# Kernel tuning notes

Hardware: AMD Instinct MI355X
Metric: run time of the kernel (lower is better)

Reference implementation:

```python
import jax, jax.numpy as jnp
import numpy as np
from jax import lax

# Model constants (match init_kwargs)
DIM = 512
NUM_HEADS = 8
HEAD_DIM = 64
INNER = NUM_HEADS * HEAD_DIM  # 512
SCALE = HEAD_DIM ** -0.5
# CoaT ConvRelPosEnc window dict {3:2, 5:3, 7:3}: head-group sizes and kernel sizes
HEAD_SPLITS = [2, 3, 3]
KSIZES = [3, 5, 7]


def _depthwise_conv(x, w, b):
    # x: [B, Cg, H, W], w: [Cg, 1, k, k] (OIHW, depthwise), b: [Cg]
    cg = x.shape[1]
    y = lax.conv_general_dilated(
        x, w, window_strides=(1, 1), padding='SAME',
        feature_group_count=cg,
        dimension_numbers=('NCHW', 'OIHW', 'NCHW'))
    return y + b[None, :, None, None]


def setup_inputs() -> dict:
    key = jax.random.key(0)
    ks = jax.random.split(key, 10)
    B, Himg, Wimg = 16, 56, 56
    N = Himg * Wimg
    x = jax.random.normal(ks[0], (B, N, DIM), dtype=jnp.float32)
    w_qkv = jax.random.normal(ks[1], (3 * INNER, DIM), dtype=jnp.float32) * 0.02
    w_proj = jax.random.normal(ks[2], (DIM, INNER), dtype=jnp.float32) * 0.02
    b_proj = jnp.zeros((DIM,), dtype=jnp.float32)
    # depthwise conv params per head group: channels = split * HEAD_DIM
    w3 = jax.random.normal(ks[3], (2 * HEAD_DIM, 1, 3, 3), dtype=jnp.float32) * 0.02
    b3 = jnp.zeros((2 * HEAD_DIM,), dtype=jnp.float32)
    w5 = jax.random.normal(ks[4], (3 * HEAD_DIM, 1, 5, 5), dtype=jnp.float32) * 0.02
    b5 = jnp.zeros((3 * HEAD_DIM,), dtype=jnp.float32)
    w7 = jax.random.normal(ks[5], (3 * HEAD_DIM, 1, 7, 7), dtype=jnp.float32) * 0.02
    b7 = jnp.zeros((3 * HEAD_DIM,), dtype=jnp.float32)
    return {"x": x, "H": Himg, "W": Wimg,
            "w_qkv": w_qkv, "w_proj": w_proj, "b_proj": b_proj,
            "w3": w3, "b3": b3, "w5": w5, "b5": b5, "w7": w7, "b7": b7}


def reference(x, H, W, w_qkv, w_proj, b_proj, w3, b3, w5, b5, w7, b7):
    B, N, C = x.shape
    h, d = NUM_HEADS, HEAD_DIM
    qkv = x @ w_qkv.T  # [B, N, 3*INNER]
    q, k, v = jnp.split(qkv, 3, axis=-1)
    # b n (h d) -> b h n d
    def to_heads(t):
        return t.reshape(B, N, h, d).transpose(0, 2, 1, 3)
    q, k, v = to_heads(q), to_heads(k), to_heads(v)
    # factorized attention: softmax(k) over sequence dim, then two batched GEMMs
    k_softmax = jax.nn.softmax(k, axis=2)
    kv = jnp.einsum('bhnk,bhnv->bhkv', k_softmax, v)          # [B,h,d,d]
    factor_att = jnp.einsum('bhnk,bhkv->bhnv', q, kv)          # [B,h,N,d]
    # ConvRelPosEnc: depthwise conv on v (as 2D map), elementwise multiply by q
    v_img = v.transpose(0, 1, 3, 2).reshape(B, h * d, H, W)    # [B, h*d, H, W]
    c0, c1 = HEAD_SPLITS[0] * d, (HEAD_SPLITS[0] + HEAD_SPLITS[1]) * d
    conv_v = jnp.concatenate([
        _depthwise_conv(v_img[:, :c0], w3, b3),
        _depthwise_conv(v_img[:, c0:c1], w5, b5),
        _depthwise_conv(v_img[:, c1:], w7, b7),
    ], axis=1)                                                 # [B, h*d, H, W]
    conv_v = conv_v.reshape(B, h, d, N).transpose(0, 1, 3, 2)  # [B,h,N,d]
    crpe = q * conv_v
    out = SCALE * factor_att + crpe                            # [B,h,N,d]
    out = out.transpose(0, 2, 1, 3).reshape(B, N, h * d)       # b h n d -> b n (h d)
    out = out @ w_proj.T + b_proj
    return out
```

## Files before the change

kernel.cpp:

```cpp
#include <hip/hip_runtime.h>
#include <hip/hip_bf16.h>
#include <cstdint>
#include <cstddef>

using u16 = unsigned short;
using u32 = unsigned int;
using f32x4 = __attribute__((ext_vector_type(4))) float;
using bf16x8 = __attribute__((ext_vector_type(8))) short;

#define NB   16
#define NSEQ 3136
#define NH   8
#define HD   64
#define CDIM 512
#define CQKV 1536

static __device__ __forceinline__ u16 f2bf(float f) {
  u32 u = __builtin_bit_cast(u32, f);
  u = (u + 0x7FFFu + ((u >> 16) & 1u)) >> 16;
  return (u16)u;
}
static __device__ __forceinline__ float bf2f(u16 h) {
  u32 u = ((u32)h) << 16;
  return __builtin_bit_cast(float, u);
}
static __device__ __forceinline__ void async16(const void* g, void* l) {
  __builtin_amdgcn_global_load_lds((const __attribute__((address_space(1))) u32*)g,
                                   (__attribute__((address_space(3))) u32*)l, 16, 0, 0);
}

__global__ __launch_bounds__(256) void cvt_kernel(const float* __restrict__ in,
                                                  u16* __restrict__ out, int n4) {
  int i = (int)(blockIdx.x * 256 + threadIdx.x);
  if (i >= n4) return;
  f32x4 v = *(const f32x4*)(in + (size_t)i * 4);
  uint2 uu;
  uu.x = (u32)f2bf(v[0]) | ((u32)f2bf(v[1]) << 16);
  uu.y = (u32)f2bf(v[2]) | ((u32)f2bf(v[3]) << 16);
  *(uint2*)(out + (size_t)i * 4) = uu;
}

#define VMW(n) asm volatile("s_waitcnt vmcnt(" #n ")" ::: "memory")

template<bool OUT_FP32>
__global__ __launch_bounds__(512, 2) void gemm256(
    const u16* __restrict__ Ap, const u16* __restrict__ Bp, void* __restrict__ Cp,
    const float* __restrict__ bias, int K, int lda, int ldb, int ldc, int nbn)
{
  __shared__ u16 sm[2][2][2][128 * 64];
  int nwg = (int)gridDim.x;
  int bid = (int)blockIdx.x;
  int wg = (bid & 7) * (nwg >> 3) + (bid >> 3);
  int bm = wg / nbn, bn = wg - bm * nbn;
  int m0 = bm * 256, n0 = bn * 256;
  int t = (int)threadIdx.x;
  int lane = t & 63, w = t >> 6;
  int wm = w >> 2, wn = w & 3;
  int lr = lane & 15, lk = (lane >> 4) * 8;

  f32x4 acc[2][2][4][2] = {};
  bf16x8 av[4][2], bv[2][2];
  const int KT = K >> 6;

  auto stage = [&](int b, int op, int half, int kt) {
    const u16* P = op ? Bp : Ap;
    int ld = op ? ldb : lda;
    int base0 = op ? n0 : m0;
    int gc = (kt << 6) + ((((t & 7) ^ ((t >> 3) & 7))) << 3);
    #pragma unroll
    for (int rd = 0; rd < 2; ++rd) {
      int gr = base0 + half * 128 + rd * 64 + (t >> 3);
      async16(P + (size_t)gr * ld + gc, &sm[b][op][half][rd * 4096 + w * 512]);
    }
  };
  auto LOADA = [&](int b, int h) {
    #pragma unroll
    for (int mi = 0; mi < 4; ++mi)
      #pragma unroll
      for (int kk = 0; kk < 2; ++kk) {
        int r = wm * 64 + mi * 16 + lr;
        int c = kk * 32 + lk;
        av[mi][kk] = *(const bf16x8*)&sm[b][0][h][r * 64 + (c ^ ((r & 7) << 3))];
      }
  };
  auto LOADB = [&](int b, int g) {
    #pragma unroll
    for (int ni = 0; ni < 2; ++ni)
      #pragma unroll
      for (int kk = 0; kk < 2; ++kk) {
        int r = wn * 32 + ni * 16 + lr;
        int c = kk * 32 + lk;
        bv[ni][kk] = *(const bf16x8*)&sm[b][1][g][r * 64 + (c ^ ((r & 7) << 3))];
      }
  };

#define BARSEQ                                                  \
  __builtin_amdgcn_s_barrier();                                 \
  asm volatile("s_waitcnt lgkmcnt(0)" ::: "memory");            \
  __builtin_amdgcn_sched_barrier(0);                            \
  __builtin_amdgcn_s_setprio(1)
#define ENDP                                                    \
  __builtin_amdgcn_s_setprio(0);                                \
  __builtin_amdgcn_s_barrier()
#define MMQ(h_, g_)                                                          \
  _Pragma("unroll")                                                          \
  for (int kk = 0; kk < 2; ++kk) {                                           \
    _Pragma("unroll")                                                        \
    for (int mi = 0; mi < 4; ++mi) {                                         \
      _Pragma("unroll")                                                      \
      for (int ni = 0; ni < 2; ++ni)                                         \
        acc[h_][g_][mi][ni] = __builtin_amdgcn_mfma_f32_16x16x32_bf16(       \
            av[mi][kk], bv[ni][kk], acc[h_][g_][mi][ni], 0, 0, 0);           \
    }                                                                        \
  }

  stage(0, 0, 0, 0); stage(0, 1, 0, 0); stage(0, 0, 1, 0); stage(0, 1, 1, 0);
  VMW(4);
  __builtin_amdgcn_s_barrier();

  for (int kt = 0; kt < KT - 1; ++kt) {
    int bb = kt & 1;
    LOADA(bb, 0); LOADB(bb, 0);
    stage(bb ^ 1, 0, 0, kt + 1);
    VMW(2);
    BARSEQ; MMQ(0, 0); ENDP;
    LOADB(bb, 1);
    stage(bb ^ 1, 1, 0, kt + 1);
    BARSEQ; MMQ(0, 1); ENDP;
    LOADA(bb, 1);
    stage(bb ^ 1, 0, 1, kt + 1);
    BARSEQ; MMQ(1, 1); ENDP;
    LOADB(bb, 0);
    stage(bb ^ 1, 1, 1, kt + 1);
    VMW(4);
    BARSEQ; MMQ(1, 0); ENDP;
  }
  {
    int bb = (KT - 1) & 1;
    LOADA(bb, 0); LOADB(bb, 0);
    VMW(0);
    BARSEQ; MMQ(0, 0); ENDP;
    LOADB(bb, 1);
    BARSEQ; MMQ(0, 1); ENDP;
    LOADA(bb, 1);
    BARSEQ; MMQ(1, 1); ENDP;
    LOADB(bb, 0);
    BARSEQ; MMQ(1, 0); ENDP;
  }
#undef MMQ
#undef BARSEQ
#undef ENDP

  if constexpr (!OUT_FP32) {
    __syncthreads();
    u16* cs = (u16*)sm;
    #pragma unroll
    for (int h = 0; h < 2; ++h)
      #pragma unroll
      for (int g = 0; g < 2; ++g)
        #pragma unroll
        for (int mi = 0; mi < 4; ++mi)
          #pragma unroll
          for (int ni = 0; ni < 2; ++ni)
            #pragma unroll
            for (int r = 0; r < 4; ++r) {
              int row = h * 128 + wm * 64 + mi * 16 + (lane >> 4) * 4 + r;
              int col = g * 128 + wn * 32 + ni * 16 + lr;
              cs[row * 256 + (col ^ (((row >> 2) & 7) << 3))] = f2bf(acc[h][g][mi][ni][r]);
            }
    __syncthreads();
    #pragma unroll
    for (int i = 0; i < 16; ++i) {
      int e = (i * 512 + t) * 8;
      int row = e >> 8, col = e & 255;
      uint4 v = *(const uint4*)&cs[row * 256 + (col ^ (((row >> 2) & 7) << 3))];
      *(uint4*)&((u16*)Cp)[(size_t)(m0 + row) * ldc + n0 + col] = v;
    }
  } else {
    float* cf = (float*)sm;
    #pragma unroll
    for (int h = 0; h < 2; ++h) {
      __syncthreads();
      #pragma unroll
      for (int g = 0; g < 2; ++g)
        #pragma unroll
        for (int mi = 0; mi < 4; ++mi)
          #pragma unroll
          for (int ni = 0; ni < 2; ++ni)
            #pragma unroll
            for (int r = 0; r < 4; ++r) {
              int row = wm * 64 + mi * 16 + (lane >> 4) * 4 + r;
              int col = g * 128 + wn * 32 + ni * 16 + lr;
              cf[row * 256 + (col ^ (((row >> 2) & 7) << 3))] = acc[h][g][mi][ni][r];
            }
      __syncthreads();
      #pragma unroll
      for (int i = 0; i < 16; ++i) {
        int e = (i * 512 + t) * 4;
        int row = e >> 8, col = e & 255;
        f32x4 v = *(const f32x4*)&cf[row * 256 + (col ^ (((row >> 2) & 7) << 3))];
        f32x4 b4 = *(const f32x4*)&bias[n0 + col];
        v += b4;
        *(f32x4*)&((float*)Cp)[(size_t)(m0 + h * 128 + row) * ldc + n0 + col] = v;
      }
    }
  }
}

__global__ __launch_bounds__(256) void kv_partial_kernel(const u16* __restrict__ qkvb,
                                                         float* __restrict__ part) {
  int bid = (int)blockIdx.x;
  int ns = bid & 7, h = (bid >> 3) & 7, b = bid >> 6;
  int t = (int)threadIdx.x;
  int lane = t & 63, w = t >> 6;
  __shared__ float ek[56 * 64];
  __shared__ u16  vv[56 * 64];
  __shared__ float mg[64 * 64];
  int dk0 = (lane >> 3) * 8, dv0 = (lane & 7) * 8;
  float acc[8][8] = {};
  float sacc = 0.f;
  int nbase = ns * 392;
  for (int c0 = 0; c0 < 392; c0 += 56) {
    __syncthreads();
    for (int idx = t; idx < 448; idx += 256) {
      int row = idx >> 3, c8 = idx & 7;
      size_t go = (size_t)(b * NSEQ + nbase + c0 + row) * CQKV + h * HD + c8 * 8;
      uint4 kq = *(const uint4*)&qkvb[go + CDIM];
      uint4 vq = *(const uint4*)&qkvb[go + 2 * CDIM];
      const u16* kp = (const u16*)&kq;
      #pragma unroll
      for (int j = 0; j < 8; ++j)
        ek[row * 64 + c8 * 8 + j] = __expf(bf2f(kp[j]));
      *(uint4*)&vv[row * 64 + c8 * 8] = vq;
    }
    __syncthreads();
    if (w == 0) {
      #pragma unroll 4
      for (int n = 0; n < 56; ++n) sacc += ek[n * 64 + lane];
    }
    for (int n = w * 14; n < w * 14 + 14; ++n) {
      f32x4 e0 = *(const f32x4*)&ek[n * 64 + dk0];
      f32x4 e1 = *(const f32x4*)&ek[n * 64 + dk0 + 4];
      bf16x8 vq = *(const bf16x8*)&vv[n * 64 + dv0];
      float vf[8];
      #pragma unroll
      for (int j = 0; j < 8; ++j) vf[j] = bf2f((u16)vq[j]);
      #pragma unroll
      for (int i = 0; i < 4; ++i)
        #pragma unroll
        for (int j = 0; j < 8; ++j) {
          acc[i][j]     += e0[i] * vf[j];
          acc[i + 4][j] += e1[i] * vf[j];
        }
    }
  }
  __syncthreads();
  for (int wi = 0; wi < 4; ++wi) {
    if (w == wi) {
      #pragma unroll
      for (int i = 0; i < 8; ++i) {
        #pragma unroll
        for (int j4 = 0; j4 < 2; ++j4) {
          f32x4* p = (f32x4*)&mg[(dk0 + i) * 64 + dv0 + j4 * 4];
          f32x4 a;
          #pragma unroll
          for (int j = 0; j < 4; ++j) a[j] = acc[i][j4 * 4 + j];
          if (wi == 0) *p = a; else *p += a;
        }
      }
    }
    __syncthreads();
  }
  float* dst = part + (size_t)((ns * 16 + b) * 8 + h) * 4160;
  for (int i4 = t; i4 < 1024; i4 += 256)
    *(f32x4*)&dst[i4 * 4] = *(const f32x4*)&mg[i4 * 4];
  if (w == 0) dst[4096 + lane] = sacc;
}

__global__ __launch_bounds__(256) void kv_reduce_kernel(const float* __restrict__ part,
                                                        float* __restrict__ kvb) {
  int idx = (int)(blockIdx.x * 256 + threadIdx.x);
  int bh = idx >> 10, e4 = idx & 1023;
  int b = bh >> 3, h = bh & 7;
  int dk = e4 >> 4;
  float s = 0.f;
  f32x4 o; o[0] = 0.f; o[1] = 0.f; o[2] = 0.f; o[3] = 0.f;
  #pragma unroll
  for (int c = 0; c < 8; ++c) {
    const float* src = part + (size_t)((c * 16 + b) * 8 + h) * 4160;
    o += *(const f32x4*)&src[e4 * 4];
    s += src[4096 + dk];
  }
  float inv = 1.0f / s;
  o *= inv;
  *(f32x4*)&kvb[(size_t)bh * 4096 + e4 * 4] = o;
}

template<int R>
__global__ __launch_bounds__(256) void conv_kernel(u16* __restrict__ qkvb,
    const float* __restrict__ w, const float* __restrict__ bias, int hbase, int nh) {
  constexpr int KS = 2 * R + 1;
  constexpr int WT = 14 + 2 * R;
  __shared__ u16 vt[WT * WT * 64];
  int bid = (int)blockIdx.x;
  int hh = bid % nh;
  int tile = (bid / nh) & 15;
  int b = bid / (nh * 16);
  int h = hbase + hh;
  int y0 = (tile >> 2) * 14, x0 = (tile & 3) * 14;
  int t = (int)threadIdx.x;
  for (int idx = t; idx < WT * WT * 8; idx += 256) {
    int pix = idx >> 3, c8 = idx & 7;
    int py = pix / WT, px = pix - py * WT;
    int gy = y0 + py - R, gx = x0 + px - R;
    uint4 val; val.x = 0u; val.y = 0u; val.z = 0u; val.w = 0u;
    if (gy >= 0 && gy < 56 && gx >= 0 && gx < 56)
      val = *(const uint4*)&qkvb[(size_t)(b * NSEQ + gy * 56 + gx) * CQKV + 2 * CDIM + h * HD + c8 * 8];
    *(uint4*)&vt[pix * 64 + c8 * 8] = val;
  }
  __syncthreads();
  int d = t & 63, g = t >> 6;
  int cg = hh * 64 + d;
  float wr[KS * KS];
  #pragma unroll
  for (int i = 0; i < KS * KS; ++i) wr[i] = w[cg * KS * KS + i];
  float bb = bias[cg];
  for (int px = g; px < 14; px += 4) {
    float acc[14];
    #pragma unroll
    for (int i = 0; i < 14; ++i) acc[i] = bb;
    #pragma unroll
    for (int iy = 0; iy < 14 + 2 * R; ++iy) {
      float val[KS];
      #pragma unroll
      for (int dx = 0; dx < KS; ++dx) val[dx] = bf2f(vt[(iy * WT + px + dx) * 64 + d]);
      #pragma unroll
      for (int dy = 0; dy < KS; ++dy) {
        int py = iy - dy;
        if (py >= 0 && py < 14) {
          #pragma unroll
          for (int dx = 0; dx < KS; ++dx) acc[py] += wr[dy * KS + dx] * val[dx];
        }
      }
    }
    #pragma unroll
    for (int py = 0; py < 14; ++py)
      qkvb[(size_t)(b * NSEQ + (y0 + py) * 56 + x0 + px) * CQKV + CDIM + h * HD + d] = f2bf(acc[py]);
  }
}

__global__ __launch_bounds__(256) void combine_kernel(u16* __restrict__ qkvb,
                                                      const float* __restrict__ kvb) {
  int bid = (int)blockIdx.x;
  int rt = bid % 49;
  int h = (bid / 49) & 7;
  int b = bid / 392;
  int n0 = rt * 64;
  int t = (int)threadIdx.x;
  int lane = t & 63, w = t >> 6;
  __shared__ u16 qs[64 * 72];
  __shared__ u16 cvs[64 * 64];
  __shared__ u16 kvT[64 * 64];

  #pragma unroll
  for (int i = 0; i < 2; ++i) {
    int idx = i * 256 + t;
    int row = idx >> 3, c8 = idx & 7;
    int srccol = (c8 ^ (row & 7)) << 3;
    size_t go = (size_t)(b * NSEQ + n0 + row) * CQKV + h * HD + srccol;
    async16(qkvb + go, &qs[idx * 8]);
    async16(qkvb + go + CDIM, &cvs[idx * 8]);
  }
  const float* kvsrc = kvb + (size_t)(b * 8 + h) * 4096;
  #pragma unroll
  for (int i = 0; i < 4; ++i) {
    int idx = i * 256 + t;
    int dk = idx & 63, dv0 = (idx >> 6) * 4;
    f32x4 v = *(const f32x4*)&kvsrc[dk * 64 + dv0];
    #pragma unroll
    for (int j = 0; j < 4; ++j) {
      int dv = dv0 + j;
      kvT[dv * 64 + ((((dk >> 3) ^ (dv & 7)) << 3) | (dk & 7))] = f2bf(v[j]);
    }
  }
  VMW(0);
  __syncthreads();

  int lr = lane & 15, lk = (lane >> 4) * 8;
  f32x4 acc[4] = {};
  bf16x8 av[2], bv[4][2];
  #pragma unroll
  for (int kk = 0; kk < 2; ++kk) {
    int r = w * 16 + lr;
    int c = kk * 32 + lk;
    av[kk] = *(const bf16x8*)&qs[r * 64 + (c ^ ((r & 7) << 3))];
  }
  #pragma unroll
  for (int ni = 0; ni < 4; ++ni)
    #pragma unroll
    for (int kk = 0; kk < 2; ++kk) {
      int r = ni * 16 + lr;
      int c = kk * 32 + lk;
      bv[ni][kk] = *(const bf16x8*)&kvT[r * 64 + (c ^ ((r & 7) << 3))];
    }
  #pragma unroll
  for (int kk = 0; kk < 2; ++kk)
    #pragma unroll
    for (int ni = 0; ni < 4; ++ni)
      acc[ni] = __builtin_amdgcn_mfma_f32_16x16x32_bf16(av[kk], bv[ni][kk], acc[ni], 0, 0, 0);

  float outv[4][4];
  #pragma unroll
  for (int ni = 0; ni < 4; ++ni)
    #pragma unroll
    for (int r = 0; r < 4; ++r) {
      int nrow = w * 16 + (lane >> 4) * 4 + r;
      int dv = ni * 16 + lr;
      int sw = ((((dv >> 3) ^ (nrow & 7)) << 3) | (dv & 7));
      float qv = bf2f(qs[nrow * 64 + sw]);
      float cv = bf2f(cvs[nrow * 64 + sw]);
      outv[ni][r] = 0.125f * acc[ni][r] + qv * cv;
    }
  __syncthreads();
  #pragma unroll
  for (int ni = 0; ni < 4; ++ni)
    #pragma unroll
    for (int r = 0; r < 4; ++r) {
      int nrow = w * 16 + (lane >> 4) * 4 + r;
      int dv = ni * 16 + lr;
      qs[nrow * 72 + dv] = f2bf(outv[ni][r]);
    }
  __syncthreads();
  {
    int row = t >> 2, c0 = (t & 3) * 16;
    uint4 x0 = *(const uint4*)&qs[row * 72 + c0];
    uint4 x1 = *(const uint4*)&qs[row * 72 + c0 + 8];
    u16* dst = &qkvb[(size_t)(b * NSEQ + n0 + row) * CQKV + h * HD + c0];
    *(uint4*)dst = x0;
    *(uint4*)&dst[8] = x1;
  }
}

extern "C" void kernel_launch(void* const* d_in, const int* in_sizes, int n_in,
                              void* d_out, int out_size, void* d_ws, size_t ws_size,
                              hipStream_t stream) {
  (void)in_sizes; (void)n_in; (void)out_size; (void)ws_size;
  const float* x      = (const float*)d_in[0];
  const float* w_qkv  = (const float*)d_in[3];
  const float* w_proj = (const float*)d_in[4];
  const float* b_proj = (const float*)d_in[5];
  const float* w3 = (const float*)d_in[6];
  const float* b3 = (const float*)d_in[7];
  const float* w5 = (const float*)d_in[8];
  const float* b5 = (const float*)d_in[9];
  const float* w7 = (const float*)d_in[10];
  const float* b7 = (const float*)d_in[11];
  float* out = (float*)d_out;

  char* ws = (char*)d_ws;
  u16* qkvb = (u16*)ws;        ws += (size_t)50176 * 1536 * 2;
  u16* wqb  = (u16*)ws;        ws += (size_t)1536 * 512 * 2;
  u16* wpb  = (u16*)ws;        ws += (size_t)512 * 512 * 2;
  float* kvpart = (float*)ws;  ws += (size_t)1024 * 4160 * 4;
  float* kvb = (float*)ws;     ws += (size_t)16 * 8 * 64 * 64 * 4;
  u16* xb = (u16*)ws;          ws += (size_t)50176 * 512 * 2;

  cvt_kernel<<<768, 256, 0, stream>>>(w_qkv, wqb, 1536 * 512 / 4);
  cvt_kernel<<<256, 256, 0, stream>>>(w_proj, wpb, 512 * 512 / 4);
  cvt_kernel<<<25088, 256, 0, stream>>>(x, xb, 50176 * 512 / 4);
  gemm256<false><<<1176, 512, 0, stream>>>(xb, wqb, qkvb, nullptr,
                                           512, 512, 512, 1536, 6);
  kv_partial_kernel<<<1024, 256, 0, stream>>>(qkvb, kvpart);
  kv_reduce_kernel<<<512, 256, 0, stream>>>(kvpart, kvb);
  conv_kernel<1><<<512, 256, 0, stream>>>(qkvb, w3, b3, 0, 2);
  conv_kernel<2><<<768, 256, 0, stream>>>(qkvb, w5, b5, 2, 3);
  conv_kernel<3><<<768, 256, 0, stream>>>(qkvb, w7, b7, 5, 3);
  combine_kernel<<<6272, 256, 0, stream>>>(qkvb, kvb);
  gemm256<true><<<392, 512, 0, stream>>>(qkvb, wpb, out, b_proj,
                                         512, 1536, 512, 512, 2);
}
```

Baseline: 320.7 us.

## Merge kv-partial and depthwise conv kernels into one interleaved launch

Replaces the kv_partial kernel and the three per-window conv kernels with one mid_kernel. Its blocks are interleaved, one kv-partial block for every two conv blocks, and share a single static shared-memory buffer. The conv output now goes to a separate buffer (reusing the xb workspace) instead of overwriting the k slot of qkv in place, which removes the write hazard between the kv and conv blocks. The goal is fewer launches and better GPU fill through overlapping heterogeneous work. The cost is that every block reserves the largest shared-memory footprint, which can lower occupancy, and combine now reads conv values from a second array.

```diff
diff --git a/kernel.cpp b/kernel.cpp
--- a/kernel.cpp
+++ b/kernel.cpp
@@ -207,15 +207,15 @@
   }
 }
 
-__global__ __launch_bounds__(256) void kv_partial_kernel(const u16* __restrict__ qkvb,
-                                                         float* __restrict__ part) {
-  int bid = (int)blockIdx.x;
+
+static __device__ __forceinline__ void kvp_body(int bid, char* smem,
+    const u16* __restrict__ qkvb, float* __restrict__ part) {
   int ns = bid & 7, h = (bid >> 3) & 7, b = bid >> 6;
   int t = (int)threadIdx.x;
   int lane = t & 63, w = t >> 6;
-  __shared__ float ek[56 * 64];
-  __shared__ u16  vv[56 * 64];
-  __shared__ float mg[64 * 64];
+  float* ek = (float*)smem;
+  u16*  vv  = (u16*)(smem + 14336);
+  float* mg = (float*)(smem + 21504);
   int dk0 = (lane >> 3) * 8, dv0 = (lane & 7) * 8;
   float acc[8][8] = {};
   float sacc = 0.f;
@@ -277,32 +277,13 @@
   if (w == 0) dst[4096 + lane] = sacc;
 }
 
-__global__ __launch_bounds__(256) void kv_reduce_kernel(const float* __restrict__ part,
-                                                        float* __restrict__ kvb) {
-  int idx = (int)(blockIdx.x * 256 + threadIdx.x);
-  int bh = idx >> 10, e4 = idx & 1023;
-  int b = bh >> 3, h = bh & 7;
-  int dk = e4 >> 4;
-  float s = 0.f;
-  f32x4 o; o[0] = 0.f; o[1] = 0.f; o[2] = 0.f; o[3] = 0.f;
-  #pragma unroll
-  for (int c = 0; c < 8; ++c) {
-    const float* src = part + (size_t)((c * 16 + b) * 8 + h) * 4160;
-    o += *(const f32x4*)&src[e4 * 4];
-    s += src[4096 + dk];
-  }
-  float inv = 1.0f / s;
-  o *= inv;
-  *(f32x4*)&kvb[(size_t)bh * 4096 + e4 * 4] = o;
-}
-
 template<int R>
-__global__ __launch_bounds__(256) void conv_kernel(u16* __restrict__ qkvb,
-    const float* __restrict__ w, const float* __restrict__ bias, int hbase, int nh) {
+static __device__ __forceinline__ void conv_body(int bid, char* smem,
+    const u16* __restrict__ qkvb, u16* __restrict__ cvout,
+    const float* __restrict__ wp, const float* __restrict__ bias, int hbase, int nh) {
   constexpr int KS = 2 * R + 1;
   constexpr int WT = 14 + 2 * R;
-  __shared__ u16 vt[WT * WT * 64];
-  int bid = (int)blockIdx.x;
+  u16* vt = (u16*)smem;
   int hh = bid % nh;
   int tile = (bid / nh) & 15;
   int b = bid / (nh * 16);
@@ -323,7 +304,7 @@
   int cg = hh * 64 + d;
   float wr[KS * KS];
   #pragma unroll
-  for (int i = 0; i < KS * KS; ++i) wr[i] = w[cg * KS * KS + i];
+  for (int i = 0; i < KS * KS; ++i) wr[i] = wp[cg * KS * KS + i];
   float bb = bias[cg];
   for (int px = g; px < 14; px += 4) {
     float acc[14];
@@ -345,11 +326,49 @@
     }
     #pragma unroll
     for (int py = 0; py < 14; ++py)
-      qkvb[(size_t)(b * NSEQ + (y0 + py) * 56 + x0 + px) * CQKV + CDIM + h * HD + d] = f2bf(acc[py]);
-  }
+      cvout[(size_t)(b * NSEQ + (y0 + py) * 56 + x0 + px) * CDIM + h * HD + d] = f2bf(acc[py]);
+  }
+}
+
+__global__ __launch_bounds__(256) void mid_kernel(const u16* __restrict__ qkvb,
+    u16* __restrict__ cvout, float* __restrict__ part,
+    const float* __restrict__ w3, const float* __restrict__ b3,
+    const float* __restrict__ w5, const float* __restrict__ b5,
+    const float* __restrict__ w7, const float* __restrict__ b7) {
+  __shared__ alignas(16) char smem[51200];
+  int bid = (int)blockIdx.x;
+  int q3 = bid / 3, r3 = bid - q3 * 3;
+  if (r3 == 0) {
+    kvp_body(q3, smem, qkvb, part);
+  } else {
+    int cid = 2 * q3 + (r3 - 1);
+    if (cid < 512)        conv_body<1>(cid,        smem, qkvb, cvout, w3, b3, 0, 2);
+    else if (cid < 1280)  conv_body<2>(cid - 512,  smem, qkvb, cvout, w5, b5, 2, 3);
+    else                  conv_body<3>(cid - 1280, smem, qkvb, cvout, w7, b7, 5, 3);
+  }
+}
+
+__global__ __launch_bounds__(256) void kv_reduce_kernel(const float* __restrict__ part,
+                                                        float* __restrict__ kvb) {
+  int idx = (int)(blockIdx.x * 256 + threadIdx.x);
+  int bh = idx >> 10, e4 = idx & 1023;
+  int b = bh >> 3, h = bh & 7;
+  int dk = e4 >> 4;
+  float s = 0.f;
+  f32x4 o; o[0] = 0.f; o[1] = 0.f; o[2] = 0.f; o[3] = 0.f;
+  #pragma unroll
+  for (int c = 0; c < 8; ++c) {
+    const float* src = part + (size_t)((c * 16 + b) * 8 + h) * 4160;
+    o += *(const f32x4*)&src[e4 * 4];
+    s += src[4096 + dk];
+  }
+  float inv = 1.0f / s;
+  o *= inv;
+  *(f32x4*)&kvb[(size_t)bh * 4096 + e4 * 4] = o;
 }
 
 __global__ __launch_bounds__(256) void combine_kernel(u16* __restrict__ qkvb,
+                                                      const u16* __restrict__ cvin,
                                                       const float* __restrict__ kvb) {
   int bid = (int)blockIdx.x;
   int rt = bid % 49;
@@ -367,9 +386,8 @@
     int idx = i * 256 + t;
     int row = idx >> 3, c8 = idx & 7;
     int srccol = (c8 ^ (row & 7)) << 3;
-    size_t go = (size_t)(b * NSEQ + n0 + row) * CQKV + h * HD + srccol;
-    async16(qkvb + go, &qs[idx * 8]);
-    async16(qkvb + go + CDIM, &cvs[idx * 8]);
+    async16(qkvb + (size_t)(b * NSEQ + n0 + row) * CQKV + h * HD + srccol, &qs[idx * 8]);
+    async16(cvin + (size_t)(b * NSEQ + n0 + row) * CDIM + h * HD + srccol, &cvs[idx * 8]);
   }
   const float* kvsrc = kvb + (size_t)(b * 8 + h) * 4096;
   #pragma unroll
@@ -470,12 +488,9 @@
   cvt_kernel<<<25088, 256, 0, stream>>>(x, xb, 50176 * 512 / 4);
   gemm256<false><<<1176, 512, 0, stream>>>(xb, wqb, qkvb, nullptr,
                                            512, 512, 512, 1536, 6);
-  kv_partial_kernel<<<1024, 256, 0, stream>>>(qkvb, kvpart);
+  mid_kernel<<<3072, 256, 0, stream>>>(qkvb, xb, kvpart, w3, b3, w5, b5, w7, b7);
   kv_reduce_kernel<<<512, 256, 0, stream>>>(kvpart, kvb);
-  conv_kernel<1><<<512, 256, 0, stream>>>(qkvb, w3, b3, 0, 2);
-  conv_kernel<2><<<768, 256, 0, stream>>>(qkvb, w5, b5, 2, 3);
-  conv_kernel<3><<<768, 256, 0, stream>>>(qkvb, w7, b7, 5, 3);
-  combine_kernel<<<6272, 256, 0, stream>>>(qkvb, kvb);
+  combine_kernel<<<6272, 256, 0, stream>>>(qkvb, xb, kvb);
   gemm256<true><<<392, 512, 0, stream>>>(qkvb, wpb, out, b_proj,
                                          512, 1536, 512, 512, 2);
 }
```

New measurement: 310.2 us. 3.3% less time.
